# Performance work log

Measured on AMD Instinct MI355X. Metric: run time of the kernel, lower is better.

The kernel has to match this reference:

```python
import jax, jax.numpy as jnp
import numpy as np

B, Z, H, D, T, L = 2048, 64, 256, 8, 250, 2


def setup_inputs() -> dict:
    key = jax.random.key(0)
    ks = jax.random.split(key, 10)
    s = 0.05  # small init scale for stable LSTM dynamics
    n = lambda k, shp, sc=1.0: jax.random.normal(k, shp, dtype=jnp.float32) * sc
    return {
        "z": n(ks[0], (B, Z)),
        "target_seq": n(ks[1], (B, T, D)),
        "fc_hidden_w": n(ks[2], (Z, H * L), s),
        "fc_hidden_b": jnp.zeros((H * L,), jnp.float32),
        "fc_cell_w": n(ks[3], (Z, H * L), s),
        "fc_cell_b": jnp.zeros((H * L,), jnp.float32),
        "W_ih0": n(ks[4], (D, 4 * H), s),
        "W_hh0": n(ks[5], (H, 4 * H), s),
        "b_ih0": jnp.zeros((4 * H,), jnp.float32),
        "b_hh0": jnp.zeros((4 * H,), jnp.float32),
        "W_ih1": n(ks[6], (H, 4 * H), s),
        "W_hh1": n(ks[7], (H, 4 * H), s),
        "b_ih1": jnp.zeros((4 * H,), jnp.float32),
        "b_hh1": jnp.zeros((4 * H,), jnp.float32),
        "fc_out_w": n(ks[8], (H, D), s),
        "fc_out_b": jnp.zeros((D,), jnp.float32),
    }


def _lstm_cell(x, h, c, Wih, Whh, bih, bhh):
    # PyTorch gate order: i, f, g, o
    gates = x @ Wih + bih + h @ Whh + bhh  # [B, 4H]
    i, f, g, o = jnp.split(gates, 4, axis=-1)
    c_new = jax.nn.sigmoid(f) * c + jax.nn.sigmoid(i) * jnp.tanh(g)
    h_new = jax.nn.sigmoid(o) * jnp.tanh(c_new)
    return h_new, c_new


def reference(z, target_seq, fc_hidden_w, fc_hidden_b, fc_cell_w, fc_cell_b,
              W_ih0, W_hh0, b_ih0, b_hh0, W_ih1, W_hh1, b_ih1, b_hh1,
              fc_out_w, fc_out_b):
    bsz = z.shape[0]
    # Faithful to torch .view(num_layers, batch, hidden) on [B, H*L] output
    h0_all = (z @ fc_hidden_w + fc_hidden_b).reshape(L, bsz, H)
    c0_all = (z @ fc_cell_w + fc_cell_b).reshape(L, bsz, H)
    # Teacher forcing ratio 1.0: input at step t is target[:, t-1] (zeros at t=0)
    first = jnp.zeros((bsz, 1, target_seq.shape[-1]), target_seq.dtype)
    inputs = jnp.concatenate([first, target_seq[:, :-1]], axis=1)  # [B, T, D]
    xs = jnp.transpose(inputs, (1, 0, 2))  # time-major [T, B, D]

    def step(carry, xt):
        h0, c0, h1, c1 = carry
        h0, c0 = _lstm_cell(xt, h0, c0, W_ih0, W_hh0, b_ih0, b_hh0)
        h1, c1 = _lstm_cell(h0, h1, c1, W_ih1, W_hh1, b_ih1, b_hh1)
        return (h0, c0, h1, c1), h1

    init = (h0_all[0], c0_all[0], h0_all[1], c0_all[1])
    _, hs = jax.lax.scan(step, init, xs)  # hs: [T, B, H]
    hs = jnp.transpose(hs, (1, 0, 2))  # [B, T, H]
    reconstructed = hs @ fc_out_w + fc_out_b  # [B, T, D]
    return reconstructed
```

## Files before the change

### kernel.cpp

```cpp
#include <hip/hip_runtime.h>
#include <cstddef>
#include <cstdint>


#define BSZ    2048
#define ZDIM   64
#define HDIM   256
#define DDIM   8
#define TSTEPS 250
#define ROWS   16
#define NWG    (BSZ / ROWS)
#define NTH    512
#define G4     1024
#define WSTR   264

typedef __attribute__((ext_vector_type(4))) int v4i;

__device__ __forceinline__ unsigned short f2bf(float x) {
  union { float f; unsigned u; } v; v.f = x;
  unsigned r = v.u + 0x7fff + ((v.u >> 16) & 1);
  return (unsigned short)(r >> 16);
}
__device__ __forceinline__ float bf2f(unsigned short b) {
  union { unsigned u; float f; } v; v.u = (unsigned)b << 16; return v.f;
}
__device__ __forceinline__ float fexp2(float x) { return __builtin_amdgcn_exp2f(x); }
__device__ __forceinline__ float frcp(float x)  { return __builtin_amdgcn_rcpf(x); }
__device__ __forceinline__ float sigm(float x)  { return frcp(1.f + fexp2(-1.44269504f * x)); }
__device__ __forceinline__ float tanh_(float x) { return 2.f * frcp(1.f + fexp2(-2.88539008f * x)) - 1.f; }
__device__ __forceinline__ char q8(float x, float s) {
  float v = fminf(fmaxf(x * s, -127.f), 127.f);
  return (char)(int)__builtin_rintf(v);
}
__device__ __forceinline__ void q8pair(float h, float s, char* hi, char* lo) {
  float hs = fminf(fmaxf(h * s, -127.f), 127.f);
  float hq = __builtin_rintf(hs);
  *hi = (char)(int)hq;
  *lo = (char)(int)__builtin_rintf((hs - hq) * 254.f);
}

__global__ void init_state(const float* __restrict__ z,
                           const float* __restrict__ Wfh, const float* __restrict__ bfh,
                           const float* __restrict__ Wfc, const float* __restrict__ bfc,
                           char* __restrict__ h0h, char* __restrict__ h0l,
                           char* __restrict__ h1h, char* __restrict__ h1l,
                           float* __restrict__ c0s, float* __restrict__ c1s)
{
  int idx = blockIdx.x * 256 + threadIdx.x;
  int b = idx >> 8;
  int j = idx & 255;
  int col = ((b & 1) << 8) | j;
  const float* z0 = z + (size_t)(b >> 1) * ZDIM;
  const float* z1 = z + (size_t)(1024 + (b >> 1)) * ZDIM;
  float h0 = bfh[col], c0v = bfc[col], h1 = bfh[col], c1v = bfc[col];
  for (int k = 0; k < ZDIM; ++k) {
    float wh = Wfh[k * 512 + col];
    float wc = Wfc[k * 512 + col];
    float a = z0[k], bb = z1[k];
    h0  += a * wh;  c0v += a * wc;
    h1  += bb * wh; c1v += bb * wc;
  }
  char hi, lo;
  q8pair(h0, 31.75f, &hi, &lo); h0h[idx] = hi; h0l[idx] = lo;
  q8pair(h1, 31.75f, &hi, &lo); h1h[idx] = hi; h1l[idx] = lo;
  c0s[idx] = c0v; c1s[idx] = c1v;
}

__global__ void col_scales(const float* __restrict__ Whh0,
                           const float* __restrict__ Wih1, const float* __restrict__ Whh1,
                           float* __restrict__ cs0, float* __restrict__ qs0,
                           float* __restrict__ cs1, float* __restrict__ qs1)
{
  int c = blockIdx.x * 256 + threadIdx.x;
  if (c < 1024) {
    float m = 0.f;
    for (int k = 0; k < 256; ++k) m = fmaxf(m, fabsf(Whh0[(size_t)k * G4 + c]));
    cs0[c] = m * (1.f / 16129.f);
    qs0[c] = 127.f / m;
  } else {
    c -= 1024;
    float m = 0.f;
    for (int k = 0; k < 256; ++k) m = fmaxf(m, fabsf(Whh1[(size_t)k * G4 + c]));
    for (int k = 0; k < 256; ++k) m = fmaxf(m, fabsf(Wih1[(size_t)k * G4 + c]));
    cs1[c] = m * (1.f / 16129.f);
    qs1[c] = 127.f / m;
  }
}

__global__ void pack_i8(const float* __restrict__ Whh0,
                        const float* __restrict__ Wih1, const float* __restrict__ Whh1,
                        const float* __restrict__ qs0, const float* __restrict__ qs1,
                        char* __restrict__ p0, char* __restrict__ p1)
{
  int tt   = blockIdx.x * 4 + (threadIdx.x >> 6);
  int lane = threadIdx.x & 63;
  int l15 = lane & 15, lq = lane >> 4;
  union { char c[16]; uint4 u; } v;
  if (tt < 256) {
    int w = tt >> 5, kc = (tt >> 3) & 3, i = tt & 7;
    int nt = (i >> 1) * 16 + 2 * w + (i & 1);
    int col = nt * 16 + l15;
    float q = qs0[col];
    for (int j = 0; j < 16; ++j) {
      int k = kc * 64 + lq * 16 + j;
      v.c[j] = q8(Whh0[(size_t)k * G4 + col], q);
    }
    *(uint4*)(p0 + (size_t)tt * 1024 + lane * 16) = v.u;
  } else {
    int t1 = tt - 256;
    int w = t1 >> 6, kc = (t1 >> 3) & 7, i = t1 & 7;
    int nt = (i >> 1) * 16 + 2 * w + (i & 1);
    int col = nt * 16 + l15;
    float q = qs1[col];
    for (int j = 0; j < 16; ++j) {
      int k = kc * 64 + lq * 16 + j;
      float wv = (k < 256) ? Whh1[(size_t)k * G4 + col]
                           : Wih1[(size_t)(k - 256) * G4 + col];
      v.c[j] = q8(wv, q);
    }
    *(uint4*)(p1 + (size_t)t1 * 1024 + lane * 16) = v.u;
  }
}

__global__ __launch_bounds__(NTH, 1) void lstm_run(
    const float* __restrict__ target,
    const char* __restrict__ p0, const char* __restrict__ p1,
    const float* __restrict__ bih0, const float* __restrict__ bhh0,
    const float* __restrict__ bih1, const float* __restrict__ bhh1,
    const float* __restrict__ Wih0,
    const float* __restrict__ Wout, const float* __restrict__ bout,
    const char* __restrict__ h0h, const char* __restrict__ h0l,
    const char* __restrict__ h1h, const char* __restrict__ h1l,
    const float* __restrict__ c0s, const float* __restrict__ c1s,
    const float* __restrict__ cs0, const float* __restrict__ cs1,
    float* __restrict__ out)
{
  __shared__ uint4 X4h[32 * 16];
  __shared__ uint4 X4l[32 * 16];
  __shared__ unsigned short h1f[16 * WSTR];
  __shared__ unsigned short woutT[8 * WSTR];
  __shared__ float x_lds[16 * 8];

  const int tid  = threadIdx.x;
  const int w    = tid >> 6;
  const int lane = tid & 63;
  const int l15  = lane & 15;
  const int lq   = lane >> 4;
  const int b0   = blockIdx.x * ROWS;
  char* Xch = (char*)X4h;
  char* Xcl = (char*)X4l;

  {
    int m = tid & 15, blk = tid >> 4;
    const char* sh = (blk < 16) ? h1h : h0h;
    const char* sl = (blk < 16) ? h1l : h0l;
    int jblk = blk & 15;
    X4h[blk * 16 + m] = *(const uint4*)(sh + (size_t)(b0 + m) * HDIM + jblk * 16);
    X4l[blk * 16 + m] = *(const uint4*)(sl + (size_t)(b0 + m) * HDIM + jblk * 16);
  }
  for (int i = tid; i < HDIM * DDIM; i += NTH) {
    int k = i >> 3, d = i & 7;
    woutT[d * WSTR + k] = f2bf(Wout[i]);
  }

  const int myrow = lq * 4;
  const int jc0   = 32 * w + l15;
  float c0r[2][4], c1r[2][4];
  float bA0[8], bA1[8], csA0[8], csA1[8];
  float wx[8][8];
#pragma unroll
  for (int i = 0; i < 8; ++i) {
    int col = (i >> 1) * 256 + jc0 + 16 * (i & 1);
    bA0[i]  = bih0[col] + bhh0[col];
    bA1[i]  = bih1[col] + bhh1[col];
    csA0[i] = cs0[col];
    csA1[i] = cs1[col];
#pragma unroll
    for (int d = 0; d < 8; ++d) wx[i][d] = Wih0[d * G4 + col];
  }
#pragma unroll
  for (int cc = 0; cc < 2; ++cc) {
    int j = jc0 + cc * 16;
#pragma unroll
    for (int r = 0; r < 4; ++r) {
      c0r[cc][r] = c0s[(size_t)(b0 + myrow + r) * HDIM + j];
      c1r[cc][r] = c1s[(size_t)(b0 + myrow + r) * HDIM + j];
    }
  }
  const int opr = tid >> 5, opd = (tid >> 2) & 7, opq = tid & 3;
  const float bo_out = bout[opd];

  const char* gp0 = p0 + (size_t)w * 32768 + lane * 16;
  const char* gp1 = p1 + (size_t)w * 65536 + lane * 16;

#define A0VH(KC) __builtin_bit_cast(v4i, X4h[(16 + (KC) * 4 + lq) * 16 + l15])
#define A0VL(KC) __builtin_bit_cast(v4i, X4l[(16 + (KC) * 4 + lq) * 16 + l15])
#define A1VH(KC) __builtin_bit_cast(v4i, X4h[((KC) * 4 + lq) * 16 + l15])
#define A1VL(KC) __builtin_bit_cast(v4i, X4l[((KC) * 4 + lq) * 16 + l15])

  v4i breg[8];
#pragma unroll
  for (int s = 0; s < 8; ++s)
    breg[s] = *(const v4i*)(gp0 + (size_t)s * 1024);

  __syncthreads();

#pragma unroll 1
  for (int t = 0; t < TSTEPS; ++t) {
    if (tid < 128) {
      int m = tid >> 3, d = tid & 7;
      x_lds[m * 8 + d] = (t == 0) ? 0.f
          : target[(size_t)(b0 + m) * (TSTEPS * DDIM) + (size_t)(t - 1) * DDIM + d];
    }
    __syncthreads();

    const float sc0 = (t <= 1) ? 4.f : 1.f;
    const float sc1 = (t == 0) ? 4.f : 1.f;
    const float wq0 = (t == 0) ? 31.75f : 127.f;

    v4i acch[8], accl[8];
    const v4i zi = {0, 0, 0, 0};

#pragma unroll
    for (int i = 0; i < 8; ++i) { acch[i] = zi; accl[i] = zi; }
    {
      v4i ah, al;
#pragma unroll 8
      for (int j = 0; j < 32; ++j) {
        const int i = j & 7;
        if (i == 0) { int kc = j >> 3; ah = A0VH(kc); al = A0VL(kc); }
        acch[i] = __builtin_amdgcn_mfma_i32_16x16x64_i8(ah, breg[i], acch[i], 0, 0, 0);
        accl[i] = __builtin_amdgcn_mfma_i32_16x16x64_i8(al, breg[i], accl[i], 0, 0, 0);
        const int jn = j + 8;
        breg[i] = (jn < 32) ? *(const v4i*)(gp0 + (size_t)jn * 1024)
                            : *(const v4i*)(gp1 + (size_t)(jn - 32) * 1024);
      }
    }
    __syncthreads();

    {
      float4 xa[4], xb[4];
#pragma unroll
      for (int r = 0; r < 4; ++r) {
        xa[r] = *(const float4*)&x_lds[(myrow + r) * 8];
        xb[r] = *(const float4*)&x_lds[(myrow + r) * 8 + 4];
      }
#pragma unroll
      for (int cc = 0; cc < 2; ++cc) {
        float gf4[4][4];
#pragma unroll
        for (int g = 0; g < 4; ++g) {
          int i = g * 2 + cc;
          float cs = csA0[i] * sc0;
#pragma unroll
          for (int r = 0; r < 4; ++r)
            gf4[g][r] = ((float)acch[i][r] + (float)accl[i][r] * (1.f / 254.f)) * cs + bA0[i];
        }
#pragma unroll
        for (int g = 0; g < 4; ++g) {
          int i = g * 2 + cc;
#pragma unroll
          for (int r = 0; r < 4; ++r)
            gf4[g][r] += xa[r].x * wx[i][0] + xa[r].y * wx[i][1]
                       + xa[r].z * wx[i][2] + xa[r].w * wx[i][3]
                       + xb[r].x * wx[i][4] + xb[r].y * wx[i][5]
                       + xb[r].z * wx[i][6] + xb[r].w * wx[i][7];
        }
#pragma unroll
        for (int r = 0; r < 4; ++r) {
          float iv = sigm(gf4[0][r]);
          float fv = sigm(gf4[1][r]);
          float gv = tanh_(gf4[2][r]);
          float ov = sigm(gf4[3][r]);
          c0r[cc][r] = fv * c0r[cc][r] + iv * gv;
          char hi, lo;
          q8pair(ov * tanh_(c0r[cc][r]), wq0, &hi, &lo);
          int off = ((16 + 2 * w + cc) * 16 + myrow + r) * 16 + l15;
          Xch[off] = hi; Xcl[off] = lo;
        }
      }
    }
    __syncthreads();

#pragma unroll
    for (int i = 0; i < 8; ++i) { acch[i] = zi; accl[i] = zi; }
    {
      v4i ah, al;
#pragma unroll 8
      for (int j = 0; j < 64; ++j) {
        const int i = j & 7;
        if (i == 0) { int kc = j >> 3; ah = A1VH(kc); al = A1VL(kc); }
        acch[i] = __builtin_amdgcn_mfma_i32_16x16x64_i8(ah, breg[i], acch[i], 0, 0, 0);
        accl[i] = __builtin_amdgcn_mfma_i32_16x16x64_i8(al, breg[i], accl[i], 0, 0, 0);
        const int jn = j + 8;
        breg[i] = (jn < 64) ? *(const v4i*)(gp1 + (size_t)jn * 1024)
                            : *(const v4i*)(gp0 + (size_t)(jn - 64) * 1024);
      }
    }
    __syncthreads();

#pragma unroll
    for (int cc = 0; cc < 2; ++cc)
#pragma unroll
      for (int r = 0; r < 4; ++r) {
        float di = ((float)acch[0 + cc][r] + (float)accl[0 + cc][r] * (1.f / 254.f));
        float df = ((float)acch[2 + cc][r] + (float)accl[2 + cc][r] * (1.f / 254.f));
        float dg = ((float)acch[4 + cc][r] + (float)accl[4 + cc][r] * (1.f / 254.f));
        float dv = ((float)acch[6 + cc][r] + (float)accl[6 + cc][r] * (1.f / 254.f));
        float iv = sigm(di * csA1[0 + cc] * sc1 + bA1[0 + cc]);
        float fv = sigm(df * csA1[2 + cc] * sc1 + bA1[2 + cc]);
        float gv = tanh_(dg * csA1[4 + cc] * sc1 + bA1[4 + cc]);
        float ov = sigm(dv * csA1[6 + cc] * sc1 + bA1[6 + cc]);
        c1r[cc][r] = fv * c1r[cc][r] + iv * gv;
        float h = ov * tanh_(c1r[cc][r]);
        char hi, lo;
        q8pair(h, 127.f, &hi, &lo);
        int off = ((2 * w + cc) * 16 + myrow + r) * 16 + l15;
        Xch[off] = hi; Xcl[off] = lo;
        h1f[(myrow + r) * WSTR + jc0 + cc * 16] = f2bf(h);
      }
    __syncthreads();

    {
      float s_ = 0.f;
#pragma unroll
      for (int i = 0; i < 16; ++i) {
        ushort4 hx = *(const ushort4*)&h1f[opr * WSTR + i * 16 + opq * 4];
        ushort4 wv = *(const ushort4*)&woutT[opd * WSTR + i * 16 + opq * 4];
        s_ += bf2f(hx.x) * bf2f(wv.x) + bf2f(hx.y) * bf2f(wv.y)
            + bf2f(hx.z) * bf2f(wv.z) + bf2f(hx.w) * bf2f(wv.w);
      }
      s_ += __shfl_xor(s_, 1);
      s_ += __shfl_xor(s_, 2);
      if (opq == 0)
        out[(size_t)(b0 + opr) * (TSTEPS * DDIM) + (size_t)t * DDIM + opd] =
            s_ + bo_out;
    }
  }
#undef A0VH
#undef A0VL
#undef A1VH
#undef A1VL
}

extern "C" void kernel_launch(void* const* d_in, const int* in_sizes, int n_in,
                              void* d_out, int out_size, void* d_ws, size_t ws_size,
                              hipStream_t stream) {
  const float* z    = (const float*)d_in[0];
  const float* tgt  = (const float*)d_in[1];
  const float* Wfh  = (const float*)d_in[2];
  const float* bfh  = (const float*)d_in[3];
  const float* Wfc  = (const float*)d_in[4];
  const float* bfc  = (const float*)d_in[5];
  const float* Wih0 = (const float*)d_in[6];
  const float* Whh0 = (const float*)d_in[7];
  const float* bih0 = (const float*)d_in[8];
  const float* bhh0 = (const float*)d_in[9];
  const float* Wih1 = (const float*)d_in[10];
  const float* Whh1 = (const float*)d_in[11];
  const float* bih1 = (const float*)d_in[12];
  const float* bhh1 = (const float*)d_in[13];
  const float* Wout = (const float*)d_in[14];
  const float* bout = (const float*)d_in[15];

  char* ws = (char*)d_ws;
  char*  p0   = ws;
  char*  p1   = ws + 262144;
  char*  h0h  = ws + 786432;
  char*  h0l  = ws + 1310720;
  char*  h1h  = ws + 1835008;
  char*  h1l  = ws + 2359296;
  float* c0s  = (float*)(ws + 2883584);
  float* c1s  = (float*)(ws + 4980736);
  float* cs0  = (float*)(ws + 7077888);
  float* qs0  = (float*)(ws + 7081984);
  float* cs1  = (float*)(ws + 7086080);
  float* qs1  = (float*)(ws + 7090176);

  hipLaunchKernelGGL(init_state, dim3(BSZ * HDIM / 256), dim3(256), 0, stream,
                     z, Wfh, bfh, Wfc, bfc, h0h, h0l, h1h, h1l, c0s, c1s);
  hipLaunchKernelGGL(col_scales, dim3(8), dim3(256), 0, stream,
                     Whh0, Wih1, Whh1, cs0, qs0, cs1, qs1);
  hipLaunchKernelGGL(pack_i8, dim3(192), dim3(256), 0, stream,
                     Whh0, Wih1, Whh1, qs0, qs1, p0, p1);
  hipLaunchKernelGGL(lstm_run, dim3(NWG), dim3(NTH), 0, stream,
                     tgt, p0, p1, bih0, bhh0, bih1, bhh1, Wih0, Wout, bout,
                     h0h, h0l, h1h, h1l, c0s, c1s, cs0, cs1, (float*)d_out);
}
```

Before: 3.075 ms.

## Double-buffer LDS hidden states to drop barriers and defer output projection

Double-buffers the int8 hidden-state LDS tiles and the bf16 h1 buffer by timestep parity, which removes three of the five __syncthreads per step. Each thread now loads its own x rows straight from global memory instead of staging them through LDS. The output projection for step t-1 moves inside step t so it overlaps with the layer-0 gate compute, and the last step is handled after the loop. This doubles LDS use for the X buffers, and correctness now relies on the parity indexing being consistent across the two layers.

```diff
diff --git a/kernel.cpp b/kernel.cpp
--- a/kernel.cpp
+++ b/kernel.cpp
@@ -135,11 +135,10 @@
     const float* __restrict__ cs0, const float* __restrict__ cs1,
     float* __restrict__ out)
 {
-  __shared__ uint4 X4h[32 * 16];
-  __shared__ uint4 X4l[32 * 16];
-  __shared__ unsigned short h1f[16 * WSTR];
+  __shared__ uint4 X4h[1024];
+  __shared__ uint4 X4l[1024];
+  __shared__ unsigned short h1f[2][16 * WSTR];
   __shared__ unsigned short woutT[8 * WSTR];
-  __shared__ float x_lds[16 * 8];
 
   const int tid  = threadIdx.x;
   const int w    = tid >> 6;
@@ -193,11 +192,6 @@
   const char* gp0 = p0 + (size_t)w * 32768 + lane * 16;
   const char* gp1 = p1 + (size_t)w * 65536 + lane * 16;
 
-#define A0VH(KC) __builtin_bit_cast(v4i, X4h[(16 + (KC) * 4 + lq) * 16 + l15])
-#define A0VL(KC) __builtin_bit_cast(v4i, X4l[(16 + (KC) * 4 + lq) * 16 + l15])
-#define A1VH(KC) __builtin_bit_cast(v4i, X4h[((KC) * 4 + lq) * 16 + l15])
-#define A1VL(KC) __builtin_bit_cast(v4i, X4l[((KC) * 4 + lq) * 16 + l15])
-
   v4i breg[8];
 #pragma unroll
   for (int s = 0; s < 8; ++s)
@@ -207,12 +201,25 @@
 
 #pragma unroll 1
   for (int t = 0; t < TSTEPS; ++t) {
-    if (tid < 128) {
-      int m = tid >> 3, d = tid & 7;
-      x_lds[m * 8 + d] = (t == 0) ? 0.f
-          : target[(size_t)(b0 + m) * (TSTEPS * DDIM) + (size_t)(t - 1) * DDIM + d];
-    }
-    __syncthreads();
+    const int xc = (t & 1) << 9;
+    const int xn = xc ^ 512;
+
+    float4 xa[4], xb[4];
+    if (t > 0) {
+      const float* xp = target + (size_t)(b0 + myrow) * (TSTEPS * DDIM)
+                               + (size_t)(t - 1) * DDIM;
+#pragma unroll
+      for (int r = 0; r < 4; ++r) {
+        xa[r] = *(const float4*)(xp + (size_t)r * (TSTEPS * DDIM));
+        xb[r] = *(const float4*)(xp + (size_t)r * (TSTEPS * DDIM) + 4);
+      }
+    } else {
+#pragma unroll
+      for (int r = 0; r < 4; ++r) {
+        xa[r] = make_float4(0.f, 0.f, 0.f, 0.f);
+        xb[r] = make_float4(0.f, 0.f, 0.f, 0.f);
+      }
+    }
 
     const float sc0 = (t <= 1) ? 4.f : 1.f;
     const float sc1 = (t == 0) ? 4.f : 1.f;
@@ -228,7 +235,12 @@
 #pragma unroll 8
       for (int j = 0; j < 32; ++j) {
         const int i = j & 7;
-        if (i == 0) { int kc = j >> 3; ah = A0VH(kc); al = A0VL(kc); }
+        if (i == 0) {
+          int kc = j >> 3;
+          int aidx = xc + (16 + kc * 4 + lq) * 16 + l15;
+          ah = __builtin_bit_cast(v4i, X4h[aidx]);
+          al = __builtin_bit_cast(v4i, X4l[aidx]);
+        }
         acch[i] = __builtin_amdgcn_mfma_i32_16x16x64_i8(ah, breg[i], acch[i], 0, 0, 0);
         accl[i] = __builtin_amdgcn_mfma_i32_16x16x64_i8(al, breg[i], accl[i], 0, 0, 0);
         const int jn = j + 8;
@@ -236,15 +248,25 @@
                             : *(const v4i*)(gp1 + (size_t)(jn - 32) * 1024);
       }
     }
-    __syncthreads();
+
+    if (t > 0) {
+      const unsigned short* hf = h1f[(t & 1) ^ 1];
+      float s_ = 0.f;
+#pragma unroll
+      for (int i = 0; i < 16; ++i) {
+        ushort4 hx = *(const ushort4*)&hf[opr * WSTR + i * 16 + opq * 4];
+        ushort4 wv = *(const ushort4*)&woutT[opd * WSTR + i * 16 + opq * 4];
+        s_ += bf2f(hx.x) * bf2f(wv.x) + bf2f(hx.y) * bf2f(wv.y)
+            + bf2f(hx.z) * bf2f(wv.z) + bf2f(hx.w) * bf2f(wv.w);
+      }
+      s_ += __shfl_xor(s_, 1);
+      s_ += __shfl_xor(s_, 2);
+      if (opq == 0)
+        out[(size_t)(b0 + opr) * (TSTEPS * DDIM) + (size_t)(t - 1) * DDIM + opd] =
+            s_ + bo_out;
+    }
 
     {
-      float4 xa[4], xb[4];
-#pragma unroll
-      for (int r = 0; r < 4; ++r) {
-        xa[r] = *(const float4*)&x_lds[(myrow + r) * 8];
-        xb[r] = *(const float4*)&x_lds[(myrow + r) * 8 + 4];
-      }
 #pragma unroll
       for (int cc = 0; cc < 2; ++cc) {
         float gf4[4][4];
@@ -275,7 +297,7 @@
           c0r[cc][r] = fv * c0r[cc][r] + iv * gv;
           char hi, lo;
           q8pair(ov * tanh_(c0r[cc][r]), wq0, &hi, &lo);
-          int off = ((16 + 2 * w + cc) * 16 + myrow + r) * 16 + l15;
+          int off = (xn + (16 + 2 * w + cc) * 16 + myrow + r) * 16 + l15;
           Xch[off] = hi; Xcl[off] = lo;
         }
       }
@@ -289,7 +311,13 @@
 #pragma unroll 8
       for (int j = 0; j < 64; ++j) {
         const int i = j & 7;
-        if (i == 0) { int kc = j >> 3; ah = A1VH(kc); al = A1VL(kc); }
+        if (i == 0) {
+          int kc = j >> 3;
+          int aidx = (kc < 4) ? (xc + (kc * 4 + lq) * 16 + l15)
+                              : (xn + (16 + (kc - 4) * 4 + lq) * 16 + l15);
+          ah = __builtin_bit_cast(v4i, X4h[aidx]);
+          al = __builtin_bit_cast(v4i, X4l[aidx]);
+        }
         acch[i] = __builtin_amdgcn_mfma_i32_16x16x64_i8(ah, breg[i], acch[i], 0, 0, 0);
         accl[i] = __builtin_amdgcn_mfma_i32_16x16x64_i8(al, breg[i], accl[i], 0, 0, 0);
         const int jn = j + 8;
@@ -297,7 +325,6 @@
                             : *(const v4i*)(gp0 + (size_t)(jn - 64) * 1024);
       }
     }
-    __syncthreads();
 
 #pragma unroll
     for (int cc = 0; cc < 2; ++cc)
@@ -315,32 +342,29 @@
         float h = ov * tanh_(c1r[cc][r]);
         char hi, lo;
         q8pair(h, 127.f, &hi, &lo);
-        int off = ((2 * w + cc) * 16 + myrow + r) * 16 + l15;
+        int off = (xn + (2 * w + cc) * 16 + myrow + r) * 16 + l15;
         Xch[off] = hi; Xcl[off] = lo;
-        h1f[(myrow + r) * WSTR + jc0 + cc * 16] = f2bf(h);
+        h1f[t & 1][(myrow + r) * WSTR + jc0 + cc * 16] = f2bf(h);
       }
     __syncthreads();
-
-    {
-      float s_ = 0.f;
-#pragma unroll
-      for (int i = 0; i < 16; ++i) {
-        ushort4 hx = *(const ushort4*)&h1f[opr * WSTR + i * 16 + opq * 4];
-        ushort4 wv = *(const ushort4*)&woutT[opd * WSTR + i * 16 + opq * 4];
-        s_ += bf2f(hx.x) * bf2f(wv.x) + bf2f(hx.y) * bf2f(wv.y)
-            + bf2f(hx.z) * bf2f(wv.z) + bf2f(hx.w) * bf2f(wv.w);
-      }
-      s_ += __shfl_xor(s_, 1);
-      s_ += __shfl_xor(s_, 2);
-      if (opq == 0)
-        out[(size_t)(b0 + opr) * (TSTEPS * DDIM) + (size_t)t * DDIM + opd] =
-            s_ + bo_out;
-    }
-  }
-#undef A0VH
-#undef A0VL
-#undef A1VH
-#undef A1VL
+  }
+
+  {
+    const unsigned short* hf = h1f[(TSTEPS - 1) & 1];
+    float s_ = 0.f;
+#pragma unroll
+    for (int i = 0; i < 16; ++i) {
+      ushort4 hx = *(const ushort4*)&hf[opr * WSTR + i * 16 + opq * 4];
+      ushort4 wv = *(const ushort4*)&woutT[opd * WSTR + i * 16 + opq * 4];
+      s_ += bf2f(hx.x) * bf2f(wv.x) + bf2f(hx.y) * bf2f(wv.y)
+          + bf2f(hx.z) * bf2f(wv.z) + bf2f(hx.w) * bf2f(wv.w);
+    }
+    s_ += __shfl_xor(s_, 1);
+    s_ += __shfl_xor(s_, 2);
+    if (opq == 0)
+      out[(size_t)(b0 + opr) * (TSTEPS * DDIM) + (size_t)(TSTEPS - 1) * DDIM + opd] =
+          s_ + bo_out;
+  }
 }
 
 extern "C" void kernel_launch(void* const* d_in, const int* in_sizes, int n_in,
```

Result: no change. 3.076 ms (+0.0%).
